# Optimization experiments

Hardware: AMD Instinct MI355X
Metric: run time of the kernel (lower is better)

Reference implementation:

```python
import jax, jax.numpy as jnp
import numpy as np

V, E, D = 50000, 800000, 128
EH, NH = 128, 128  # edge_hidden, node_hidden


def setup_inputs() -> dict:
    key = jax.random.key(0)
    ks = jax.random.split(key, 12)
    h = jax.random.normal(ks[0], (V, D), dtype=jnp.float32)
    edge_index = jax.random.randint(ks[1], (2, E), 0, V, dtype=jnp.int64)
    s = 0.02
    # edge MLP: Linear(2D->EH), Linear(EH->EH), Linear(EH->NH)
    W1 = jax.random.normal(ks[2], (2 * D, EH), dtype=jnp.float32) * s
    b1 = jnp.zeros((EH,), dtype=jnp.float32)
    W2 = jax.random.normal(ks[3], (EH, EH), dtype=jnp.float32) * s
    b2 = jnp.zeros((EH,), dtype=jnp.float32)
    W3 = jax.random.normal(ks[4], (EH, NH), dtype=jnp.float32) * s
    b3 = jnp.zeros((NH,), dtype=jnp.float32)
    # node MLP: Linear(D+NH->NH), Linear(NH->NH)
    Wn1 = jax.random.normal(ks[5], (D + NH, NH), dtype=jnp.float32) * s
    bn1 = jnp.zeros((NH,), dtype=jnp.float32)
    Wn2 = jax.random.normal(ks[6], (NH, NH), dtype=jnp.float32) * s
    bn2 = jnp.zeros((NH,), dtype=jnp.float32)
    return {"h": h, "edge_index": edge_index, "W1": W1, "b1": b1, "W2": W2,
            "b2": b2, "W3": W3, "b3": b3, "Wn1": Wn1, "bn1": bn1,
            "Wn2": Wn2, "bn2": bn2}


def reference(h, edge_index, W1, b1, W2, b2, W3, b3, Wn1, bn1, Wn2, bn2):
    src, dst = edge_index[0], edge_index[1]
    # gather node pairs -> edge features (E, 2D)
    edge_feat = jnp.concatenate([h[src], h[dst]], axis=-1)
    # 3-layer edge MLP
    m = jax.nn.relu(edge_feat @ W1 + b1)
    m = jax.nn.relu(m @ W2 + b2)
    messages = m @ W3 + b3                       # (E, NH)
    # scatter-add into destination nodes
    agg = jax.ops.segment_sum(messages, dst, num_segments=h.shape[0])  # (V, NH)
    # node MLP on [h, agg]
    x = jnp.concatenate([h, agg], axis=-1)       # (V, D+NH)
    out = jax.nn.relu(x @ Wn1 + bn1) @ Wn2 + bn2  # (V, NH)
    return out
```

## Files before the change

kernel.cpp:

```cpp
#include <hip/hip_runtime.h>

#define NV 50000
#define NE 800000
#define CVT_N 1600000
#define TR_N  81920
#define W3N_N 16384
#define B3N_N 128
#define NB1 49
#define NB_PERM 3125
#define NB_H1 196

typedef _Float16 f16x8 __attribute__((ext_vector_type(8)));
typedef _Float16 f16x4 __attribute__((ext_vector_type(4)));
typedef float    f32x4 __attribute__((ext_vector_type(4)));

static __device__ __forceinline__ f32x4 mfma16(f16x8 a, f16x8 b, f32x4 c) {
  return __builtin_amdgcn_mfma_f32_16x16x32_f16(a, b, c, 0, 0, 0);
}

__global__ void prep_kernel(const float* __restrict__ h, _Float16* __restrict__ hf,
    const float* __restrict__ W1, const float* __restrict__ W2, const float* __restrict__ W3,
    const float* __restrict__ Wn1, const float* __restrict__ Wn2, const float* __restrict__ b3,
    _Float16* __restrict__ w1st, _Float16* __restrict__ w1dt, _Float16* __restrict__ w2t,
    _Float16* __restrict__ wn1c, _Float16* __restrict__ wn2t, float* __restrict__ b3n,
    const int* __restrict__ ei, int* __restrict__ counts)
{
  int i = blockIdx.x * blockDim.x + threadIdx.x;
  if (i < CVT_N) {
    f32x4 v = reinterpret_cast<const f32x4*>(h)[i];
    f16x4 o;
    o[0] = (_Float16)v[0]; o[1] = (_Float16)v[1]; o[2] = (_Float16)v[2]; o[3] = (_Float16)v[3];
    reinterpret_cast<f16x4*>(hf)[i] = o;
    return;
  }
  i -= CVT_N;
  if (i < TR_N) {
    int seg = i >> 14;
    int j = i & 16383;
    int f = j >> 7, k = j & 127;
    switch (seg) {
      case 0: w1st[j] = (_Float16)W1[k * 128 + f]; break;
      case 1: w1dt[j] = (_Float16)W1[(k + 128) * 128 + f]; break;
      case 2: w2t[j]  = (_Float16)W2[k * 128 + f]; break;
      case 3: wn1c[f * 256 + k] = (_Float16)Wn1[k * 128 + f]; break;
      case 4: wn2t[j] = (_Float16)Wn2[k * 128 + f]; break;
    }
    return;
  }
  i -= TR_N;
  if (i < W3N_N) {
    int f = i >> 7, ii = i & 127;
    float a = 0.f;
    for (int j = 0; j < 128; j++) a += W3[ii * 128 + j] * Wn1[(128 + j) * 128 + f];
    wn1c[f * 256 + 128 + ii] = (_Float16)a;
    return;
  }
  i -= W3N_N;
  if (i < B3N_N) {
    float a = 0.f;
    for (int j = 0; j < 128; j++) a += b3[j] * Wn1[(128 + j) * 128 + i];
    b3n[i] = a;
    return;
  }
  i -= B3N_N;
  if (i < NE) atomicAdd(&counts[ei[NE + i]], 1);
}

__global__ __launch_bounds__(1024)
void bsum_kernel(const int* __restrict__ counts, int* __restrict__ bsum) {
  __shared__ int red[1024];
  const int t = threadIdx.x;
  int i = blockIdx.x * 1024 + t;
  red[t] = (i < NV) ? counts[i] : 0;
  __syncthreads();
  for (int off = 512; off > 0; off >>= 1) {
    if (t < off) red[t] += red[t + off];
    __syncthreads();
  }
  if (t == 0) bsum[blockIdx.x] = red[0];
}

__global__ __launch_bounds__(1024)
void offs_kernel(const int* __restrict__ counts, const int* __restrict__ bsum,
                 int* __restrict__ offsets, int* __restrict__ cursor) {
  __shared__ int s[1024];
  __shared__ int sbase;
  const int t = threadIdx.x;
  int i = blockIdx.x * 1024 + t;
  int v = (i < NV) ? counts[i] : 0;
  s[t] = v;
  if (t < 64) {
    int x = (t < blockIdx.x) ? bsum[t] : 0;
    for (int off = 1; off < 64; off <<= 1) x += __shfl_xor(x, off);
    if (t == 0) sbase = x;
  }
  __syncthreads();
  for (int off = 1; off < 1024; off <<= 1) {
    int x = (t >= off) ? s[t - off] : 0;
    __syncthreads();
    s[t] += x;
    __syncthreads();
  }
  if (i < NV) {
    int excl = sbase + s[t] - v;
    offsets[i] = excl;
    cursor[i] = excl;
    if (i == NV - 1) offsets[NV] = sbase + s[t];
  }
}

static __device__ __forceinline__ void gemm128_rows(
    const _Float16* __restrict__ hf, const int* nid, const _Float16* __restrict__ At,
    const float* __restrict__ bias, _Float16* __restrict__ Out,
    int nbase, int l15, int quad)
{
  f32x4 acc[8][4];
#pragma unroll
  for (int mt = 0; mt < 8; mt++)
#pragma unroll
    for (int nt = 0; nt < 4; nt++)
      acc[mt][nt] = (f32x4){0.f, 0.f, 0.f, 0.f};

  f16x8 Bc[4], Bn[4];
#pragma unroll
  for (int nt = 0; nt < 4; nt++)
    Bc[nt] = *reinterpret_cast<const f16x8*>(hf + (long long)nid[nt] * 128 + quad * 8);
#pragma unroll
  for (int s = 0; s < 4; s++) {
    if (s < 3) {
#pragma unroll
      for (int nt = 0; nt < 4; nt++)
        Bn[nt] = *reinterpret_cast<const f16x8*>(hf + (long long)nid[nt] * 128 + (s + 1) * 32 + quad * 8);
    }
    const int k = s * 32 + quad * 8;
#pragma unroll
    for (int mt = 0; mt < 8; mt++) {
      f16x8 A = *reinterpret_cast<const f16x8*>(At + (mt * 16 + l15) * 128 + k);
#pragma unroll
      for (int nt = 0; nt < 4; nt++)
        acc[mt][nt] = mfma16(A, Bc[nt], acc[mt][nt]);
    }
#pragma unroll
    for (int nt = 0; nt < 4; nt++) Bc[nt] = Bn[nt];
  }
#pragma unroll
  for (int mt = 0; mt < 8; mt++) {
    f32x4 bb = bias ? *reinterpret_cast<const f32x4*>(bias + mt * 16 + quad * 4)
                    : (f32x4){0.f, 0.f, 0.f, 0.f};
#pragma unroll
    for (int nt = 0; nt < 4; nt++) {
      int n = nbase + nt * 16 + l15;
      if (n < NV) {
        f16x4 o;
#pragma unroll
        for (int r = 0; r < 4; r++) o[r] = (_Float16)(acc[mt][nt][r] + bb[r]);
        *reinterpret_cast<f16x4*>(Out + (long long)n * 128 + mt * 16 + quad * 4) = o;
      }
    }
  }
}

__global__ __launch_bounds__(256, 2)
void h1p_kernel(const _Float16* __restrict__ hf, const float* __restrict__ b1,
                const _Float16* __restrict__ w1st, const _Float16* __restrict__ w1dt,
                _Float16* __restrict__ H1s, _Float16* __restrict__ H1d,
                const int* __restrict__ ei, int* __restrict__ cursor,
                int2* __restrict__ pairs)
{
  int bx = blockIdx.x;
  if (bx < NB_PERM) {
    int e = bx * 256 + threadIdx.x;
    int s = ei[e], d = ei[NE + e];
    int pos = atomicAdd(&cursor[d], 1);
    pairs[pos] = make_int2(s, d);
    return;
  }
  bx -= NB_PERM;
  const int by = bx & 1;
  const int bxx = bx >> 1;
  const int t = threadIdx.x;
  const int lane = t & 63, wave = t >> 6;
  const int quad = lane >> 4, l15 = lane & 15;
  const int nbase = bxx * 256 + wave * 64;
  int nid[4];
#pragma unroll
  for (int nt = 0; nt < 4; nt++) {
    int n = nbase + nt * 16 + l15;
    nid[nt] = n < NV ? n : NV - 1;
  }
  if (by == 0) gemm128_rows(hf, nid, w1st, nullptr, H1s, nbase, l15, quad);
  else         gemm128_rows(hf, nid, w1dt, b1,      H1d, nbase, l15, quad);
}

__global__ __launch_bounds__(128, 2)
void edge_kernel(const _Float16* __restrict__ H1s, const _Float16* __restrict__ H1d,
                 const int2* __restrict__ pairs,
                 const _Float16* __restrict__ w2t, const float* __restrict__ b2,
                 float* __restrict__ agg2)
{
  __shared__ __align__(16) _Float16 M2t[64 * 128];
  __shared__ int sdst[128];
  __shared__ int segdst[128];
  __shared__ __align__(8) unsigned char sseg8[128];
  __shared__ unsigned long long wmask[2];
  __shared__ int snbr[2];

  const int t = threadIdx.x;
  const int lane = t & 63, wave = t >> 6;
  const int quad = lane >> 4, l15 = lane & 15;
  const int ebase = blockIdx.x * 128;
  const int wbase = wave * 64;

  { int2 pr = pairs[ebase + t]; sdst[t] = pr.y; }
  if (t == 0) snbr[0] = (ebase > 0) ? pairs[ebase - 1].y : -1;
  if (t == 1) snbr[1] = (ebase + 128 < NE) ? pairs[ebase + 128].y : -1;

  int esrc[4], edst[4];
#pragma unroll
  for (int et = 0; et < 4; et++) {
    int2 pr = pairs[ebase + wbase + et * 16 + l15];
    esrc[et] = pr.x; edst[et] = pr.y;
  }

  f16x8 m1f[4][4];
#pragma unroll
  for (int et = 0; et < 4; et++) {
#pragma unroll
    for (int s = 0; s < 4; s++) {
      f16x8 a = *reinterpret_cast<const f16x8*>(H1s + (long long)esrc[et] * 128 + s * 32 + quad * 8);
      f16x8 b = *reinterpret_cast<const f16x8*>(H1d + (long long)edst[et] * 128 + s * 32 + quad * 8);
      f16x8 o = a + b;
#pragma unroll
      for (int j = 0; j < 8; j++) o[j] = o[j] > (_Float16)0 ? o[j] : (_Float16)0;
      m1f[et][s] = o;
    }
  }

  __syncthreads();
  {
    bool flag = (t > 0) && (sdst[t] != sdst[t - 1]);
    unsigned long long bm = __ballot(flag);
    if (lane == 0) wmask[wave] = bm;
    int pre = __popcll(bm & ((1ull << lane) - 1ull)) + (flag ? 1 : 0);
    __syncthreads();
    int sid = pre + (wave ? (int)__popcll(wmask[0]) : 0);
    sseg8[t] = (unsigned char)sid;
    if (flag || t == 0) segdst[sid] = sdst[t];
  }
  const int nseg = (int)__popcll(wmask[0]) + (int)__popcll(wmask[1]) + 1;
  const int nmt = (nseg + 15) >> 4;
  const bool openL = (sdst[0] == snbr[0]);
  const bool openR = (sdst[127] == snbr[1]);

  for (int half = 0; half < 2; half++) {
    f32x4 acc[4][4];
#pragma unroll
    for (int et = 0; et < 4; et++)
#pragma unroll
      for (int ft = 0; ft < 4; ft++)
        acc[et][ft] = (f32x4){0.f, 0.f, 0.f, 0.f};

#pragma unroll
    for (int s = 0; s < 4; s++) {
      const int k = s * 32 + quad * 8;
#pragma unroll
      for (int ft = 0; ft < 4; ft++) {
        f16x8 B = *reinterpret_cast<const f16x8*>(w2t + ((half * 4 + ft) * 16 + l15) * 128 + k);
#pragma unroll
        for (int et = 0; et < 4; et++)
          acc[et][ft] = mfma16(m1f[et][s], B, acc[et][ft]);
      }
    }
#pragma unroll
    for (int ft = 0; ft < 4; ft++) {
      const float bv = b2[(half * 4 + ft) * 16 + l15];
#pragma unroll
      for (int et = 0; et < 4; et++) {
        const int g = wave * 16 + et * 4 + quad;
        f16x4 o;
#pragma unroll
        for (int r = 0; r < 4; r++) {
          float x = acc[et][ft][r] + bv;
          o[r] = (_Float16)(x > 0.f ? x : 0.f);
        }
        *reinterpret_cast<f16x4*>(&M2t[(ft * 16 + l15) * 128 + ((g ^ (l15 << 1)) * 4)]) = o;
      }
    }
    __syncthreads();

    f16x8 Bf[2][4];
#pragma unroll
    for (int fl = 0; fl < 2; fl++) {
      const int flr = (wave * 2 + fl) * 16 + l15;
#pragma unroll
      for (int s = 0; s < 4; s++) {
        const int g0 = s * 8 + quad * 2;
        Bf[fl][s] = *reinterpret_cast<const f16x8*>(&M2t[flr * 128 + ((g0 ^ (l15 << 1)) * 4)]);
      }
    }
    unsigned long long segb[4];
#pragma unroll
    for (int s = 0; s < 4; s++)
      segb[s] = *reinterpret_cast<const unsigned long long*>(&sseg8[s * 32 + quad * 8]);
    __syncthreads();

    for (int mt = 0; mt < nmt; mt++) {
      const int myseg = mt * 16 + l15;
      f32x4 racc[2];
#pragma unroll
      for (int fl = 0; fl < 2; fl++) racc[fl] = (f32x4){0.f, 0.f, 0.f, 0.f};
#pragma unroll
      for (int s = 0; s < 4; s++) {
        f16x8 S;
#pragma unroll
        for (int j = 0; j < 8; j++)
          S[j] = ((int)((segb[s] >> (8 * j)) & 255ull) == myseg) ? (_Float16)1 : (_Float16)0;
#pragma unroll
        for (int fl = 0; fl < 2; fl++)
          racc[fl] = mfma16(S, Bf[fl][s], racc[fl]);
      }
#pragma unroll
      for (int fl = 0; fl < 2; fl++) {
        const int f = half * 64 + (wave * 2 + fl) * 16 + l15;
#pragma unroll
        for (int r = 0; r < 4; r++) {
          const int sg = mt * 16 + quad * 4 + r;
          if (sg < nseg) {
            float v = racc[fl][r];
            float* p = agg2 + (long long)segdst[sg] * 128 + f;
            const bool at = (sg == 0 && openL) || (sg == nseg - 1 && openR);
            if (at) unsafeAtomicAdd(p, v); else *p = v;
          }
        }
      }
    }
  }
}

__global__ __launch_bounds__(256, 2)
void node_kernel(const _Float16* __restrict__ hf, const float* __restrict__ agg2,
                 const int* __restrict__ offsets,
                 const _Float16* __restrict__ wn1c, const float* __restrict__ bn1,
                 const float* __restrict__ b3n,
                 const _Float16* __restrict__ wn2t, const float* __restrict__ bn2,
                 float* __restrict__ out)
{
  __shared__ __align__(16) _Float16 M[256 * 128];
  const int t = threadIdx.x;
  const int lane = t & 63, wave = t >> 6;
  const int quad = lane >> 4, l15 = lane & 15;
  const int wbase = wave * 64;
  const int nbase = blockIdx.x * 256 + wbase;

  int nid[4]; float fcnt[4];
#pragma unroll
  for (int nt = 0; nt < 4; nt++) {
    int n = nbase + nt * 16 + l15;
    nid[nt] = n < NV ? n : NV - 1;
    fcnt[nt] = (n < NV) ? (float)(offsets[n + 1] - offsets[n]) : 0.f;
  }

  f32x4 acc[8][4];
#pragma unroll
  for (int mt = 0; mt < 8; mt++)
#pragma unroll
    for (int nt = 0; nt < 4; nt++)
      acc[mt][nt] = (f32x4){0.f, 0.f, 0.f, 0.f};

  f16x8 Bc[4], Bn[4];
#pragma unroll
  for (int nt = 0; nt < 4; nt++)
    Bc[nt] = *reinterpret_cast<const f16x8*>(hf + (long long)nid[nt] * 128 + quad * 8);
#pragma unroll
  for (int s = 0; s < 8; s++) {
    if (s < 7) {
      const int sn = s + 1;
      if (sn < 4) {
#pragma unroll
        for (int nt = 0; nt < 4; nt++)
          Bn[nt] = *reinterpret_cast<const f16x8*>(hf + (long long)nid[nt] * 128 + sn * 32 + quad * 8);
      } else {
#pragma unroll
        for (int nt = 0; nt < 4; nt++) {
          const float* ap = agg2 + (long long)nid[nt] * 128 + (sn - 4) * 32 + quad * 8;
          f32x4 a0 = *reinterpret_cast<const f32x4*>(ap);
          f32x4 a1 = *reinterpret_cast<const f32x4*>(ap + 4);
          f16x8 bb;
#pragma unroll
          for (int j = 0; j < 4; j++) { bb[j] = (_Float16)a0[j]; bb[4 + j] = (_Float16)a1[j]; }
          Bn[nt] = bb;
        }
      }
    }
    const int k = s * 32 + quad * 8;
#pragma unroll
    for (int mt = 0; mt < 8; mt++) {
      f16x8 A = *reinterpret_cast<const f16x8*>(wn1c + (mt * 16 + l15) * 256 + k);
#pragma unroll
      for (int nt = 0; nt < 4; nt++)
        acc[mt][nt] = mfma16(A, Bc[nt], acc[mt][nt]);
    }
#pragma unroll
    for (int nt = 0; nt < 4; nt++) Bc[nt] = Bn[nt];
  }
#pragma unroll
  for (int mt = 0; mt < 8; mt++) {
    f32x4 bb  = *reinterpret_cast<const f32x4*>(bn1 + mt * 16 + quad * 4);
    f32x4 b3c = *reinterpret_cast<const f32x4*>(b3n + mt * 16 + quad * 4);
    const int cbase = 2 * mt + (quad >> 1);
#pragma unroll
    for (int nt = 0; nt < 4; nt++) {
      int row = wbase + nt * 16 + l15;
      int c = cbase ^ (row & 15);
      f16x4 o;
#pragma unroll
      for (int r = 0; r < 4; r++) {
        float x = acc[mt][nt][r] + bb[r] + fcnt[nt] * b3c[r];
        o[r] = (_Float16)(x > 0.f ? x : 0.f);
      }
      *reinterpret_cast<f16x4*>(&M[row * 128 + c * 8 + (quad & 1) * 4]) = o;
      acc[mt][nt] = (f32x4){0.f, 0.f, 0.f, 0.f};
    }
  }

#pragma unroll
  for (int s = 0; s < 4; s++) {
    f16x8 B[4];
#pragma unroll
    for (int nt = 0; nt < 4; nt++) {
      int row = wbase + nt * 16 + l15;
      B[nt] = *reinterpret_cast<const f16x8*>(&M[row * 128 + (((4 * s + quad) ^ (row & 15)) * 8)]);
    }
    const int k = s * 32 + quad * 8;
#pragma unroll
    for (int mt = 0; mt < 8; mt++) {
      f16x8 A = *reinterpret_cast<const f16x8*>(wn2t + (mt * 16 + l15) * 128 + k);
#pragma unroll
      for (int nt = 0; nt < 4; nt++)
        acc[mt][nt] = mfma16(A, B[nt], acc[mt][nt]);
    }
  }
#pragma unroll
  for (int mt = 0; mt < 8; mt++) {
    f32x4 bias = *reinterpret_cast<const f32x4*>(bn2 + mt * 16 + quad * 4);
#pragma unroll
    for (int nt = 0; nt < 4; nt++) {
      int n = nbase + nt * 16 + l15;
      if (n < NV) {
        f32x4 v;
#pragma unroll
        for (int r = 0; r < 4; r++) v[r] = acc[mt][nt][r] + bias[r];
        *reinterpret_cast<f32x4*>(out + (long long)n * 128 + mt * 16 + quad * 4) = v;
      }
    }
  }
}

static inline size_t align16(size_t x) { return (x + 15) & ~(size_t)15; }

extern "C" void kernel_launch(void* const* d_in, const int* in_sizes, int n_in,
                              void* d_out, int out_size, void* d_ws, size_t ws_size,
                              hipStream_t stream)
{
  const float* h   = (const float*)d_in[0];
  const int*   ei  = (const int*)d_in[1];
  const float* W1  = (const float*)d_in[2];
  const float* b1  = (const float*)d_in[3];
  const float* W2  = (const float*)d_in[4];
  const float* b2  = (const float*)d_in[5];
  const float* W3  = (const float*)d_in[6];
  const float* b3  = (const float*)d_in[7];
  const float* Wn1 = (const float*)d_in[8];
  const float* bn1 = (const float*)d_in[9];
  const float* Wn2 = (const float*)d_in[10];
  const float* bn2 = (const float*)d_in[11];
  float* out = (float*)d_out;

  char* p = (char*)d_ws;
  _Float16* hf   = (_Float16*)p; p += align16((size_t)NV * 128 * 2);
  _Float16* H1s  = (_Float16*)p; p += align16((size_t)NV * 128 * 2);
  _Float16* H1d  = (_Float16*)p; p += align16((size_t)NV * 128 * 2);
  _Float16* w1st = (_Float16*)p; p += align16(128 * 128 * 2);
  _Float16* w1dt = (_Float16*)p; p += align16(128 * 128 * 2);
  _Float16* w2t  = (_Float16*)p; p += align16(128 * 128 * 2);
  _Float16* wn1c = (_Float16*)p; p += align16(128 * 256 * 2);
  _Float16* wn2t = (_Float16*)p; p += align16(128 * 128 * 2);
  float*  b3n  = (float*)p;  p += align16(128 * 4);
  int* counts  = (int*)p; p += align16((size_t)NV * 4);
  int* offsets = (int*)p; p += align16((size_t)(NV + 1) * 4);
  int* cursor  = (int*)p; p += align16((size_t)NV * 4);
  int* bsum    = (int*)p; p += align16((size_t)(NB1 + 1) * 4);
  int2* pairs  = (int2*)p; p += align16((size_t)NE * 8);
  float* agg2  = (float*)p; p += align16((size_t)NV * 128 * 4);

  hipMemsetAsync(counts, 0, (size_t)NV * 4, stream);
  hipMemsetAsync(agg2, 0, (size_t)NV * 128 * 4, stream);
  {
    int total = CVT_N + TR_N + W3N_N + B3N_N + NE;
    prep_kernel<<<(total + 255) / 256, 256, 0, stream>>>(
        h, hf, W1, W2, W3, Wn1, Wn2, b3,
        w1st, w1dt, w2t, wn1c, wn2t, b3n, ei, counts);
  }
  bsum_kernel<<<NB1, 1024, 0, stream>>>(counts, bsum);
  offs_kernel<<<NB1, 1024, 0, stream>>>(counts, bsum, offsets, cursor);
  h1p_kernel<<<NB_PERM + 2 * NB_H1, 256, 0, stream>>>(hf, b1, w1st, w1dt, H1s, H1d,
                                                      ei, cursor, pairs);
  edge_kernel<<<NE / 128, 128, 0, stream>>>(H1s, H1d, pairs, w2t, b2, agg2);
  node_kernel<<<(NV + 255) / 256, 256, 0, stream>>>(hf, agg2, offsets, wn1c, bn1, b3n,
                                                    wn2t, bn2, out);
}
```

Baseline: 365.2 us.

## Split edge work across four waves per 64-edge tile and shrink node/h1 blocks

The edge kernel now processes 64 edges per 256-thread block, with each of the four waves computing a 32-feature slice of the second layer. Segment detection becomes a single-wave ballot and the two-half loop with its extra barriers goes away. The h1 and node kernels switch to 128-thread blocks, which doubles their grid counts, smaller LDS in node_kernel may raise occupancy. In exchange, every wave in an edge block redundantly gathers all 64 edges' H1 rows, and smaller tiles mean more blocks and more boundary atomics.

```diff
diff --git a/kernel.cpp b/kernel.cpp
--- a/kernel.cpp
+++ b/kernel.cpp
@@ -7,8 +7,9 @@
 #define W3N_N 16384
 #define B3N_N 128
 #define NB1 49
-#define NB_PERM 3125
-#define NB_H1 196
+#define NB_PERM 6250
+#define NB_H1 391
+#define NB_NODE 391
 
 typedef _Float16 f16x8 __attribute__((ext_vector_type(8)));
 typedef _Float16 f16x4 __attribute__((ext_vector_type(4)));
@@ -160,7 +161,7 @@
   }
 }
 
-__global__ __launch_bounds__(256, 2)
+__global__ __launch_bounds__(128, 2)
 void h1p_kernel(const _Float16* __restrict__ hf, const float* __restrict__ b1,
                 const _Float16* __restrict__ w1st, const _Float16* __restrict__ w1dt,
                 _Float16* __restrict__ H1s, _Float16* __restrict__ H1d,
@@ -169,7 +170,7 @@
 {
   int bx = blockIdx.x;
   if (bx < NB_PERM) {
-    int e = bx * 256 + threadIdx.x;
+    int e = bx * 128 + threadIdx.x;
     int s = ei[e], d = ei[NE + e];
     int pos = atomicAdd(&cursor[d], 1);
     pairs[pos] = make_int2(s, d);
@@ -181,7 +182,7 @@
   const int t = threadIdx.x;
   const int lane = t & 63, wave = t >> 6;
   const int quad = lane >> 4, l15 = lane & 15;
-  const int nbase = bxx * 256 + wave * 64;
+  const int nbase = bxx * 128 + wave * 64;
   int nid[4];
 #pragma unroll
   for (int nt = 0; nt < 4; nt++) {
@@ -192,34 +193,43 @@
   else         gemm128_rows(hf, nid, w1dt, b1,      H1d, nbase, l15, quad);
 }
 
-__global__ __launch_bounds__(128, 2)
+__global__ __launch_bounds__(256, 2)
 void edge_kernel(const _Float16* __restrict__ H1s, const _Float16* __restrict__ H1d,
                  const int2* __restrict__ pairs,
                  const _Float16* __restrict__ w2t, const float* __restrict__ b2,
                  float* __restrict__ agg2)
 {
-  __shared__ __align__(16) _Float16 M2t[64 * 128];
-  __shared__ int sdst[128];
-  __shared__ int segdst[128];
-  __shared__ __align__(8) unsigned char sseg8[128];
-  __shared__ unsigned long long wmask[2];
-  __shared__ int snbr[2];
+  __shared__ __align__(16) _Float16 M2t[128 * 64];
+  __shared__ int segdst[64];
+  __shared__ __align__(8) unsigned char sseg8[64];
 
   const int t = threadIdx.x;
   const int lane = t & 63, wave = t >> 6;
   const int quad = lane >> 4, l15 = lane & 15;
-  const int ebase = blockIdx.x * 128;
-  const int wbase = wave * 64;
-
-  { int2 pr = pairs[ebase + t]; sdst[t] = pr.y; }
-  if (t == 0) snbr[0] = (ebase > 0) ? pairs[ebase - 1].y : -1;
-  if (t == 1) snbr[1] = (ebase + 128 < NE) ? pairs[ebase + 128].y : -1;
+  const int ebase = blockIdx.x * 64;
+
+  const int2 pr = pairs[ebase + lane];
+  const int dprev = (lane > 0) ? pairs[ebase + lane - 1].y : -1;
+  const bool flag = (lane > 0) && (pr.y != dprev);
+  const unsigned long long bm = __ballot(flag);
+  const int sid = (int)__popcll(bm & ((1ull << lane) - 1ull)) + (flag ? 1 : 0);
+  if (wave == 0) {
+    sseg8[lane] = (unsigned char)sid;
+    if (flag || lane == 0) segdst[sid] = pr.y;
+  }
+  const int nseg = (int)__popcll(bm) + 1;
+  const int nmt = (nseg + 15) >> 4;
+  int prevy = -1, nexty = -1;
+  if (ebase > 0) prevy = pairs[ebase - 1].y;
+  if (ebase + 64 < NE) nexty = pairs[ebase + 64].y;
+  const bool openL = (__shfl(pr.y, 0) == prevy);
+  const bool openR = (__shfl(pr.y, 63) == nexty);
 
   int esrc[4], edst[4];
 #pragma unroll
   for (int et = 0; et < 4; et++) {
-    int2 pr = pairs[ebase + wbase + et * 16 + l15];
-    esrc[et] = pr.x; edst[et] = pr.y;
+    int2 q = pairs[ebase + et * 16 + l15];
+    esrc[et] = q.x; edst[et] = q.y;
   }
 
   f16x8 m1f[4][4];
@@ -236,108 +246,90 @@
     }
   }
 
+  f32x4 acc[4][2];
+#pragma unroll
+  for (int et = 0; et < 4; et++)
+#pragma unroll
+    for (int ft = 0; ft < 2; ft++)
+      acc[et][ft] = (f32x4){0.f, 0.f, 0.f, 0.f};
+
+#pragma unroll
+  for (int s = 0; s < 4; s++) {
+    const int k = s * 32 + quad * 8;
+#pragma unroll
+    for (int ft = 0; ft < 2; ft++) {
+      f16x8 B = *reinterpret_cast<const f16x8*>(w2t + ((wave * 2 + ft) * 16 + l15) * 128 + k);
+#pragma unroll
+      for (int et = 0; et < 4; et++)
+        acc[et][ft] = mfma16(m1f[et][s], B, acc[et][ft]);
+    }
+  }
+#pragma unroll
+  for (int ft = 0; ft < 2; ft++) {
+    const float bv = b2[(wave * 2 + ft) * 16 + l15];
+    const int f = (wave * 2 + ft) * 16 + l15;
+#pragma unroll
+    for (int et = 0; et < 4; et++) {
+      const int g = et * 4 + quad;
+      f16x4 o;
+#pragma unroll
+      for (int r = 0; r < 4; r++) {
+        float x = acc[et][ft][r] + bv;
+        o[r] = (_Float16)(x > 0.f ? x : 0.f);
+      }
+      *reinterpret_cast<f16x4*>(&M2t[f * 64 + ((g ^ ((l15 & 7) << 1)) * 4)]) = o;
+    }
+  }
   __syncthreads();
-  {
-    bool flag = (t > 0) && (sdst[t] != sdst[t - 1]);
-    unsigned long long bm = __ballot(flag);
-    if (lane == 0) wmask[wave] = bm;
-    int pre = __popcll(bm & ((1ull << lane) - 1ull)) + (flag ? 1 : 0);
-    __syncthreads();
-    int sid = pre + (wave ? (int)__popcll(wmask[0]) : 0);
-    sseg8[t] = (unsigned char)sid;
-    if (flag || t == 0) segdst[sid] = sdst[t];
-  }
-  const int nseg = (int)__popcll(wmask[0]) + (int)__popcll(wmask[1]) + 1;
-  const int nmt = (nseg + 15) >> 4;
-  const bool openL = (sdst[0] == snbr[0]);
-  const bool openR = (sdst[127] == snbr[1]);
-
-  for (int half = 0; half < 2; half++) {
-    f32x4 acc[4][4];
-#pragma unroll
-    for (int et = 0; et < 4; et++)
-#pragma unroll
-      for (int ft = 0; ft < 4; ft++)
-        acc[et][ft] = (f32x4){0.f, 0.f, 0.f, 0.f};
-
-#pragma unroll
-    for (int s = 0; s < 4; s++) {
-      const int k = s * 32 + quad * 8;
-#pragma unroll
-      for (int ft = 0; ft < 4; ft++) {
-        f16x8 B = *reinterpret_cast<const f16x8*>(w2t + ((half * 4 + ft) * 16 + l15) * 128 + k);
-#pragma unroll
-        for (int et = 0; et < 4; et++)
-          acc[et][ft] = mfma16(m1f[et][s], B, acc[et][ft]);
-      }
-    }
-#pragma unroll
-    for (int ft = 0; ft < 4; ft++) {
-      const float bv = b2[(half * 4 + ft) * 16 + l15];
-#pragma unroll
-      for (int et = 0; et < 4; et++) {
-        const int g = wave * 16 + et * 4 + quad;
-        f16x4 o;
-#pragma unroll
-        for (int r = 0; r < 4; r++) {
-          float x = acc[et][ft][r] + bv;
-          o[r] = (_Float16)(x > 0.f ? x : 0.f);
-        }
-        *reinterpret_cast<f16x4*>(&M2t[(ft * 16 + l15) * 128 + ((g ^ (l15 << 1)) * 4)]) = o;
-      }
-    }
-    __syncthreads();
-
-    f16x8 Bf[2][4];
+
+  f16x8 Bf[2][2];
+#pragma unroll
+  for (int fl = 0; fl < 2; fl++) {
+    const int f = (wave * 2 + fl) * 16 + l15;
+#pragma unroll
+    for (int s = 0; s < 2; s++) {
+      const int g0 = s * 8 + quad * 2;
+      Bf[fl][s] = *reinterpret_cast<const f16x8*>(&M2t[f * 64 + ((g0 ^ ((l15 & 7) << 1)) * 4)]);
+    }
+  }
+  unsigned long long segb[2];
+#pragma unroll
+  for (int s = 0; s < 2; s++)
+    segb[s] = *reinterpret_cast<const unsigned long long*>(&sseg8[s * 32 + quad * 8]);
+
+  for (int mt = 0; mt < nmt; mt++) {
+    const int myseg = mt * 16 + l15;
+    f32x4 racc[2];
+#pragma unroll
+    for (int fl = 0; fl < 2; fl++) racc[fl] = (f32x4){0.f, 0.f, 0.f, 0.f};
+#pragma unroll
+    for (int s = 0; s < 2; s++) {
+      f16x8 S;
+#pragma unroll
+      for (int j = 0; j < 8; j++)
+        S[j] = ((int)((segb[s] >> (8 * j)) & 255ull) == myseg) ? (_Float16)1 : (_Float16)0;
+#pragma unroll
+      for (int fl = 0; fl < 2; fl++)
+        racc[fl] = mfma16(S, Bf[fl][s], racc[fl]);
+    }
 #pragma unroll
     for (int fl = 0; fl < 2; fl++) {
-      const int flr = (wave * 2 + fl) * 16 + l15;
-#pragma unroll
-      for (int s = 0; s < 4; s++) {
-        const int g0 = s * 8 + quad * 2;
-        Bf[fl][s] = *reinterpret_cast<const f16x8*>(&M2t[flr * 128 + ((g0 ^ (l15 << 1)) * 4)]);
-      }
-    }
-    unsigned long long segb[4];
-#pragma unroll
-    for (int s = 0; s < 4; s++)
-      segb[s] = *reinterpret_cast<const unsigned long long*>(&sseg8[s * 32 + quad * 8]);
-    __syncthreads();
-
-    for (int mt = 0; mt < nmt; mt++) {
-      const int myseg = mt * 16 + l15;
-      f32x4 racc[2];
-#pragma unroll
-      for (int fl = 0; fl < 2; fl++) racc[fl] = (f32x4){0.f, 0.f, 0.f, 0.f};
-#pragma unroll
-      for (int s = 0; s < 4; s++) {
-        f16x8 S;
-#pragma unroll
-        for (int j = 0; j < 8; j++)
-          S[j] = ((int)((segb[s] >> (8 * j)) & 255ull) == myseg) ? (_Float16)1 : (_Float16)0;
-#pragma unroll
-        for (int fl = 0; fl < 2; fl++)
-          racc[fl] = mfma16(S, Bf[fl][s], racc[fl]);
-      }
-#pragma unroll
-      for (int fl = 0; fl < 2; fl++) {
-        const int f = half * 64 + (wave * 2 + fl) * 16 + l15;
-#pragma unroll
-        for (int r = 0; r < 4; r++) {
-          const int sg = mt * 16 + quad * 4 + r;
-          if (sg < nseg) {
-            float v = racc[fl][r];
-            float* p = agg2 + (long long)segdst[sg] * 128 + f;
-            const bool at = (sg == 0 && openL) || (sg == nseg - 1 && openR);
-            if (at) unsafeAtomicAdd(p, v); else *p = v;
-          }
+      const int f = (wave * 2 + fl) * 16 + l15;
+#pragma unroll
+      for (int r = 0; r < 4; r++) {
+        const int sg = mt * 16 + quad * 4 + r;
+        if (sg < nseg) {
+          float v = racc[fl][r];
+          float* p = agg2 + (long long)segdst[sg] * 128 + f;
+          const bool at = (sg == 0 && openL) || (sg == nseg - 1 && openR);
+          if (at) unsafeAtomicAdd(p, v); else *p = v;
         }
       }
     }
   }
 }
 
-__global__ __launch_bounds__(256, 2)
+__global__ __launch_bounds__(128, 2)
 void node_kernel(const _Float16* __restrict__ hf, const float* __restrict__ agg2,
                  const int* __restrict__ offsets,
                  const _Float16* __restrict__ wn1c, const float* __restrict__ bn1,
@@ -345,12 +337,12 @@
                  const _Float16* __restrict__ wn2t, const float* __restrict__ bn2,
                  float* __restrict__ out)
 {
-  __shared__ __align__(16) _Float16 M[256 * 128];
+  __shared__ __align__(16) _Float16 M[128 * 128];
   const int t = threadIdx.x;
   const int lane = t & 63, wave = t >> 6;
   const int quad = lane >> 4, l15 = lane & 15;
   const int wbase = wave * 64;
-  const int nbase = blockIdx.x * 256 + wbase;
+  const int nbase = blockIdx.x * 128 + wbase;
 
   int nid[4]; float fcnt[4];
 #pragma unroll
@@ -503,9 +495,9 @@
   }
   bsum_kernel<<<NB1, 1024, 0, stream>>>(counts, bsum);
   offs_kernel<<<NB1, 1024, 0, stream>>>(counts, bsum, offsets, cursor);
-  h1p_kernel<<<NB_PERM + 2 * NB_H1, 256, 0, stream>>>(hf, b1, w1st, w1dt, H1s, H1d,
+  h1p_kernel<<<NB_PERM + 2 * NB_H1, 128, 0, stream>>>(hf, b1, w1st, w1dt, H1s, H1d,
                                                       ei, cursor, pairs);
-  edge_kernel<<<NE / 128, 128, 0, stream>>>(H1s, H1d, pairs, w2t, b2, agg2);
-  node_kernel<<<(NV + 255) / 256, 256, 0, stream>>>(hf, agg2, offsets, wn1c, bn1, b3n,
-                                                    wn2t, bn2, out);
-}
+  edge_kernel<<<NE / 64, 256, 0, stream>>>(H1s, H1d, pairs, w2t, b2, agg2);
+  node_kernel<<<NB_NODE, 128, 0, stream>>>(hf, agg2, offsets, wn1c, bn1, b3n,
+                                           wn2t, bn2, out);
+}
```

After: 438.8 us. 20.2% more time.

## Stage per-segment H1d rows in LDS and process all 128 features in one pass

Applied to the files above, without the earlier changes.

The edge kernel now computes segment ids per wave directly from registers, which removes the initial barrier and the shared sdst array. For the first SCAP distinct destinations in each wave, it copies the H1d row into LDS once, so edges that share a destination stop re-reading that row from global memory. The two-half loop over output features is folded into one pass with twice the accumulators and a 128x128 LDS tile. This removes one barrier pair and one reduction loop per block, at the cost of much higher register pressure and LDS use, which may lower occupancy.

```diff
diff --git a/kernel.cpp b/kernel.cpp
--- a/kernel.cpp
+++ b/kernel.cpp
@@ -9,6 +9,7 @@
 #define NB1 49
 #define NB_PERM 3125
 #define NB_H1 196
+#define SCAP 12
 
 typedef _Float16 f16x8 __attribute__((ext_vector_type(8)));
 typedef _Float16 f16x4 __attribute__((ext_vector_type(4)));
@@ -198,12 +199,12 @@
                  const _Float16* __restrict__ w2t, const float* __restrict__ b2,
                  float* __restrict__ agg2)
 {
-  __shared__ __align__(16) _Float16 M2t[64 * 128];
-  __shared__ int sdst[128];
-  __shared__ int segdst[128];
+  __shared__ __align__(16) _Float16 M2t[128 * 128];
+  __shared__ __align__(16) _Float16 H1ds[2 * SCAP][136];
+  __shared__ int segdst2[2][64];
   __shared__ __align__(8) unsigned char sseg8[128];
   __shared__ unsigned long long wmask[2];
-  __shared__ int snbr[2];
+  __shared__ int snbr[4];
 
   const int t = threadIdx.x;
   const int lane = t & 63, wave = t >> 6;
@@ -211,126 +212,160 @@
   const int ebase = blockIdx.x * 128;
   const int wbase = wave * 64;
 
-  { int2 pr = pairs[ebase + t]; sdst[t] = pr.y; }
-  if (t == 0) snbr[0] = (ebase > 0) ? pairs[ebase - 1].y : -1;
-  if (t == 1) snbr[1] = (ebase + 128 < NE) ? pairs[ebase + 128].y : -1;
-
-  int esrc[4], edst[4];
+  const int2 prt = pairs[ebase + t];
+  const int dprev = (t > 0) ? pairs[ebase + t - 1].y : -1;
+  if (t == 0)   snbr[0] = (ebase > 0) ? pairs[ebase - 1].y : -1;
+  if (t == 1)   snbr[1] = (ebase + 128 < NE) ? pairs[ebase + 128].y : -1;
+  if (t == 0)   snbr[2] = prt.y;
+  if (t == 127) snbr[3] = prt.y;
+
+  const bool flag = (t > 0) && (prt.y != dprev);
+  const unsigned long long bm = __ballot(flag);
+  if (lane == 0) wmask[wave] = bm;
+  const int pre = (int)__popcll(bm & ((1ull << lane) - 1ull)) + (flag ? 1 : 0);
+  sseg8[t] = (unsigned char)pre;
+  if (flag || lane == 0) segdst2[wave][pre] = prt.y;
+
+  int esrc[4], edst[4], lsid[4];
 #pragma unroll
   for (int et = 0; et < 4; et++) {
-    int2 pr = pairs[ebase + wbase + et * 16 + l15];
-    esrc[et] = pr.x; edst[et] = pr.y;
-  }
+    int2 q = pairs[ebase + wbase + et * 16 + l15];
+    esrc[et] = q.x; edst[et] = q.y;
+    lsid[et] = __shfl(pre, et * 16 + l15);
+  }
+
+  f16x8 h1r[4][4];
+#pragma unroll
+  for (int et = 0; et < 4; et++)
+#pragma unroll
+    for (int s = 0; s < 4; s++)
+      h1r[et][s] = *reinterpret_cast<const f16x8*>(H1s + (long long)esrc[et] * 128 + s * 32 + quad * 8);
+
+  if ((flag || lane == 0) && pre < SCAP) {
+    const _Float16* src = H1d + (long long)prt.y * 128;
+    _Float16* drow = &H1ds[wave * SCAP + pre][0];
+#pragma unroll
+    for (int b = 0; b < 2; b++) {
+      f16x8 tmp[8];
+#pragma unroll
+      for (int c = 0; c < 8; c++)
+        tmp[c] = *reinterpret_cast<const f16x8*>(src + (b * 8 + c) * 8);
+#pragma unroll
+      for (int c = 0; c < 8; c++)
+        *reinterpret_cast<f16x8*>(drow + (b * 8 + c) * 8) = tmp[c];
+    }
+  }
+  asm volatile("s_waitcnt lgkmcnt(0)" ::: "memory");
+  __builtin_amdgcn_sched_barrier(0);
 
   f16x8 m1f[4][4];
 #pragma unroll
   for (int et = 0; et < 4; et++) {
+    const int ls = lsid[et];
+    const bool useL = ls < SCAP;
+    const _Float16* lrow = &H1ds[wave * SCAP + (useL ? ls : 0)][0];
+    const _Float16* grow = H1d + (long long)edst[et] * 128;
 #pragma unroll
     for (int s = 0; s < 4; s++) {
-      f16x8 a = *reinterpret_cast<const f16x8*>(H1s + (long long)esrc[et] * 128 + s * 32 + quad * 8);
-      f16x8 b = *reinterpret_cast<const f16x8*>(H1d + (long long)edst[et] * 128 + s * 32 + quad * 8);
-      f16x8 o = a + b;
+      f16x8 b;
+      if (useL) b = *reinterpret_cast<const f16x8*>(lrow + s * 32 + quad * 8);
+      else      b = *reinterpret_cast<const f16x8*>(grow + s * 32 + quad * 8);
+      f16x8 o = h1r[et][s] + b;
 #pragma unroll
       for (int j = 0; j < 8; j++) o[j] = o[j] > (_Float16)0 ? o[j] : (_Float16)0;
       m1f[et][s] = o;
     }
   }
 
+  float b2v[8];
+#pragma unroll
+  for (int ft = 0; ft < 8; ft++) b2v[ft] = b2[ft * 16 + l15];
+
+  f32x4 acc[4][8];
+#pragma unroll
+  for (int et = 0; et < 4; et++)
+#pragma unroll
+    for (int ft = 0; ft < 8; ft++)
+      acc[et][ft] = (f32x4){0.f, 0.f, 0.f, 0.f};
+
+#pragma unroll
+  for (int s = 0; s < 4; s++) {
+    const int k = s * 32 + quad * 8;
+#pragma unroll
+    for (int ft = 0; ft < 8; ft++) {
+      f16x8 B = *reinterpret_cast<const f16x8*>(w2t + (ft * 16 + l15) * 128 + k);
+#pragma unroll
+      for (int et = 0; et < 4; et++)
+        acc[et][ft] = mfma16(m1f[et][s], B, acc[et][ft]);
+    }
+  }
+#pragma unroll
+  for (int et = 0; et < 4; et++) {
+    const int g = wave * 16 + et * 4 + quad;
+#pragma unroll
+    for (int ft = 0; ft < 8; ft++) {
+      const int f = ft * 16 + l15;
+      f16x4 o;
+#pragma unroll
+      for (int r = 0; r < 4; r++) {
+        float x = acc[et][ft][r] + b2v[ft];
+        o[r] = (_Float16)(x > 0.f ? x : 0.f);
+      }
+      *reinterpret_cast<f16x4*>(&M2t[f * 128 + ((g ^ (l15 << 1)) * 4)]) = o;
+    }
+  }
   __syncthreads();
-  {
-    bool flag = (t > 0) && (sdst[t] != sdst[t - 1]);
-    unsigned long long bm = __ballot(flag);
-    if (lane == 0) wmask[wave] = bm;
-    int pre = __popcll(bm & ((1ull << lane) - 1ull)) + (flag ? 1 : 0);
-    __syncthreads();
-    int sid = pre + (wave ? (int)__popcll(wmask[0]) : 0);
-    sseg8[t] = (unsigned char)sid;
-    if (flag || t == 0) segdst[sid] = sdst[t];
-  }
-  const int nseg = (int)__popcll(wmask[0]) + (int)__popcll(wmask[1]) + 1;
+
+  const int c0 = (int)__popcll(wmask[0]);
+  const int c1 = (int)__popcll(wmask[1]);
+  const int nseg = c0 + c1 + 1;
   const int nmt = (nseg + 15) >> 4;
-  const bool openL = (sdst[0] == snbr[0]);
-  const bool openR = (sdst[127] == snbr[1]);
-
-  for (int half = 0; half < 2; half++) {
-    f32x4 acc[4][4];
-#pragma unroll
-    for (int et = 0; et < 4; et++)
-#pragma unroll
-      for (int ft = 0; ft < 4; ft++)
-        acc[et][ft] = (f32x4){0.f, 0.f, 0.f, 0.f};
-
+  const bool openL = (snbr[2] == snbr[0]);
+  const bool openR = (snbr[3] == snbr[1]);
+
+  f16x8 Bf[4][4];
+#pragma unroll
+  for (int fl = 0; fl < 4; fl++) {
+    const int f = (wave * 4 + fl) * 16 + l15;
 #pragma unroll
     for (int s = 0; s < 4; s++) {
-      const int k = s * 32 + quad * 8;
-#pragma unroll
-      for (int ft = 0; ft < 4; ft++) {
-        f16x8 B = *reinterpret_cast<const f16x8*>(w2t + ((half * 4 + ft) * 16 + l15) * 128 + k);
-#pragma unroll
-        for (int et = 0; et < 4; et++)
-          acc[et][ft] = mfma16(m1f[et][s], B, acc[et][ft]);
-      }
-    }
-#pragma unroll
-    for (int ft = 0; ft < 4; ft++) {
-      const float bv = b2[(half * 4 + ft) * 16 + l15];
-#pragma unroll
-      for (int et = 0; et < 4; et++) {
-        const int g = wave * 16 + et * 4 + quad;
-        f16x4 o;
-#pragma unroll
-        for (int r = 0; r < 4; r++) {
-          float x = acc[et][ft][r] + bv;
-          o[r] = (_Float16)(x > 0.f ? x : 0.f);
-        }
-        *reinterpret_cast<f16x4*>(&M2t[(ft * 16 + l15) * 128 + ((g ^ (l15 << 1)) * 4)]) = o;
-      }
-    }
-    __syncthreads();
-
-    f16x8 Bf[2][4];
-#pragma unroll
-    for (int fl = 0; fl < 2; fl++) {
-      const int flr = (wave * 2 + fl) * 16 + l15;
-#pragma unroll
-      for (int s = 0; s < 4; s++) {
-        const int g0 = s * 8 + quad * 2;
-        Bf[fl][s] = *reinterpret_cast<const f16x8*>(&M2t[flr * 128 + ((g0 ^ (l15 << 1)) * 4)]);
-      }
-    }
-    unsigned long long segb[4];
-#pragma unroll
-    for (int s = 0; s < 4; s++)
-      segb[s] = *reinterpret_cast<const unsigned long long*>(&sseg8[s * 32 + quad * 8]);
-    __syncthreads();
-
-    for (int mt = 0; mt < nmt; mt++) {
-      const int myseg = mt * 16 + l15;
-      f32x4 racc[2];
-#pragma unroll
-      for (int fl = 0; fl < 2; fl++) racc[fl] = (f32x4){0.f, 0.f, 0.f, 0.f};
-#pragma unroll
-      for (int s = 0; s < 4; s++) {
-        f16x8 S;
-#pragma unroll
-        for (int j = 0; j < 8; j++)
-          S[j] = ((int)((segb[s] >> (8 * j)) & 255ull) == myseg) ? (_Float16)1 : (_Float16)0;
-#pragma unroll
-        for (int fl = 0; fl < 2; fl++)
-          racc[fl] = mfma16(S, Bf[fl][s], racc[fl]);
-      }
-#pragma unroll
-      for (int fl = 0; fl < 2; fl++) {
-        const int f = half * 64 + (wave * 2 + fl) * 16 + l15;
-#pragma unroll
-        for (int r = 0; r < 4; r++) {
-          const int sg = mt * 16 + quad * 4 + r;
-          if (sg < nseg) {
-            float v = racc[fl][r];
-            float* p = agg2 + (long long)segdst[sg] * 128 + f;
-            const bool at = (sg == 0 && openL) || (sg == nseg - 1 && openR);
-            if (at) unsafeAtomicAdd(p, v); else *p = v;
-          }
+      const int g0 = s * 8 + quad * 2;
+      Bf[fl][s] = *reinterpret_cast<const f16x8*>(&M2t[f * 128 + ((g0 ^ (l15 << 1)) * 4)]);
+    }
+  }
+  unsigned long long segb[4];
+#pragma unroll
+  for (int s = 0; s < 4; s++)
+    segb[s] = *reinterpret_cast<const unsigned long long*>(&sseg8[s * 32 + quad * 8]);
+
+  for (int mt = 0; mt < nmt; mt++) {
+    const int myseg = mt * 16 + l15;
+    f32x4 racc[4];
+#pragma unroll
+    for (int fl = 0; fl < 4; fl++) racc[fl] = (f32x4){0.f, 0.f, 0.f, 0.f};
+#pragma unroll
+    for (int s = 0; s < 4; s++) {
+      const int target = myseg - ((s >= 2) ? c0 : 0);
+      f16x8 S;
+#pragma unroll
+      for (int j = 0; j < 8; j++)
+        S[j] = ((int)((segb[s] >> (8 * j)) & 255ull) == target) ? (_Float16)1 : (_Float16)0;
+#pragma unroll
+      for (int fl = 0; fl < 4; fl++)
+        racc[fl] = mfma16(S, Bf[fl][s], racc[fl]);
+    }
+#pragma unroll
+    for (int fl = 0; fl < 4; fl++) {
+      const int f = (wave * 4 + fl) * 16 + l15;
+#pragma unroll
+      for (int r = 0; r < 4; r++) {
+        const int sg = mt * 16 + quad * 4 + r;
+        if (sg < nseg) {
+          float v = racc[fl][r];
+          const int dst = (sg <= c0) ? segdst2[0][sg] : segdst2[1][sg - c0];
+          float* p = agg2 + (long long)dst * 128 + f;
+          const bool at = (sg == 0 && openL) || (sg == nseg - 1 && openR);
+          if (at) unsafeAtomicAdd(p, v); else *p = v;
         }
       }
     }
```

Result: slower. 379.0 us (+3.8%).
